# Optimization experiments

Measured on AMD Instinct MI355X. Metric: run time of the kernel, lower is better.

Reference implementation:

```python
import jax, jax.numpy as jnp
import numpy as np

B, C, N, H = 16, 256, 2048, 128


def setup_inputs() -> dict:
    key = jax.random.key(0)
    ks = jax.random.split(key, 9)
    s_in = 1.0 / np.sqrt(C)
    s_h = 1.0 / np.sqrt(H)
    return {
        "x": jax.random.normal(ks[0], (B, C, N), dtype=jnp.float32),
        "Wq": jax.random.uniform(ks[1], (H, C), jnp.float32, -s_in, s_in),
        "bq": jax.random.uniform(ks[2], (H,), jnp.float32, -s_in, s_in),
        "Wk": jax.random.uniform(ks[3], (H, C), jnp.float32, -s_in, s_in),
        "bk": jax.random.uniform(ks[4], (H,), jnp.float32, -s_in, s_in),
        "Wv": jax.random.uniform(ks[5], (H, C), jnp.float32, -s_in, s_in),
        "bv": jax.random.uniform(ks[6], (H,), jnp.float32, -s_in, s_in),
        "Wf": jax.random.uniform(ks[7], (C, H), jnp.float32, -s_h, s_h),
        "bf": jax.random.uniform(ks[8], (C,), jnp.float32, -s_h, s_h),
    }


def reference(x, Wq, bq, Wk, bk, Wv, bv, Wf, bf):
    # 1x1 conv == channel-wise linear: [B,C,N] -> [B,H,N]
    Q = jnp.einsum("bcn,hc->bhn", x, Wq) + bq[:, None]
    K = jnp.einsum("bcn,hc->bhn", x, Wk) + bk[:, None]
    V = jnp.einsum("bcn,hc->bhn", x, Wv) + bv[:, None]
    # attn[b, i, j] = softmax_j( Q[b,:,i] . K[b,:,j] )   (no sqrt(d) scaling, as in source)
    scores = jnp.einsum("bhi,bhj->bij", Q, K)          # [B, N, N]
    attn = jax.nn.softmax(scores, axis=-1)
    # out[b, h, i] = sum_j V[b,h,j] * attn[b,i,j]
    out = jnp.einsum("bhj,bij->bhi", V, attn)           # [B, H, N]
    out = jnp.einsum("bhn,ch->bcn", out, Wf) + bf[:, None]
    return out + x
```

## Files before the change

kernel.cpp:

```cpp
#include <hip/hip_runtime.h>
#include <hip/hip_bf16.h>

#define BATCH 16
#define CDIM 256
#define NDIM 2048
#define HDIM 128
#define KVB 64
#define NT (NDIM / KVB)

typedef __bf16 bf16;
typedef float f32x4 __attribute__((ext_vector_type(4)));
typedef float f32x16 __attribute__((ext_vector_type(16)));
typedef bf16 bf16x8 __attribute__((ext_vector_type(8)));
typedef unsigned int u32x4 __attribute__((ext_vector_type(4)));

#define LOG2E 1.4426950408889634f

__device__ __forceinline__ int swz512(int row, int colbyte) {
  return row * 512 + (colbyte ^ ((row & 15) << 4));
}
__device__ __forceinline__ int swz256(int row, int colbyte) {
  return row * 256 + (colbyte ^ ((row & 7) << 4));
}

__device__ __forceinline__ f32x4 mfma16(bf16x8 a, bf16x8 b, f32x4 c) {
  return __builtin_amdgcn_mfma_f32_16x16x32_bf16(a, b, c, 0, 0, 0);
}
__device__ __forceinline__ f32x16 mfma32(bf16x8 a, bf16x8 b, f32x16 c) {
  return __builtin_amdgcn_mfma_f32_32x32x16_bf16(a, b, c, 0, 0, 0);
}

__device__ __forceinline__ unsigned cvtpk(float lo, float hi) {
  unsigned r;
  asm("v_cvt_pk_bf16_f32 %0, %1, %2" : "=v"(r) : "v"(lo), "v"(hi));
  return r;
}
__device__ __forceinline__ void pswap(unsigned &a, unsigned &b) {
  asm volatile("v_permlane32_swap_b32 %0, %1" : "+v"(a), "+v"(b));
}

__device__ __forceinline__ void gload16(const bf16* g, char* l) {
  __builtin_amdgcn_global_load_lds(
      (const __attribute__((address_space(1))) void*)g,
      (__attribute__((address_space(3))) void*)l, 16, 0, 0);
}

__device__ __forceinline__ bf16x8 cvt8(float4 a, float4 b) {
  bf16x8 o;
  o[0] = (bf16)a.x; o[1] = (bf16)a.y; o[2] = (bf16)a.z; o[3] = (bf16)a.w;
  o[4] = (bf16)b.x; o[5] = (bf16)b.y; o[6] = (bf16)b.z; o[7] = (bf16)b.w;
  return o;
}

__global__ __launch_bounds__(256) void k1_qkv(
    const float* __restrict__ x,
    const float* __restrict__ Wq, const float* __restrict__ bq,
    const float* __restrict__ Wk, const float* __restrict__ bk,
    const float* __restrict__ Wv, const float* __restrict__ bv,
    bf16* __restrict__ Qo, bf16* __restrict__ Ko, bf16* __restrict__ Vo) {
  __shared__ char lds[65536];
  char* xT = lds;
  char* Wt = lds + 32768;

  const int t = threadIdx.x;
  const int l = t & 63;
  const int w = t >> 6;
  const int b = blockIdx.x >> 5;
  const int n0 = (blockIdx.x & 31) * 64;

#pragma unroll
  for (int pass = 0; pass < 16; ++pass) {
    int c = pass * 16 + (t >> 4);
    int nq = t & 15;
    const float4 v = *reinterpret_cast<const float4*>(
        x + (size_t)(b * CDIM + c) * NDIM + n0 + nq * 4);
    float fv[4] = {v.x, v.y, v.z, v.w};
#pragma unroll
    for (int i = 0; i < 4; ++i) {
      int row = nq * 4 + i;
      *reinterpret_cast<bf16*>(xT + swz512(row, c * 2)) = (bf16)fv[i];
    }
  }

  const float* Wp[3] = {Wq, Wk, Wv};
  const float* bp[3] = {bq, bk, bv};

#pragma unroll 1
  for (int p = 0; p < 3; ++p) {
    f32x4 acc[8];
#pragma unroll
    for (int i = 0; i < 8; ++i) acc[i] = f32x4{0.f, 0.f, 0.f, 0.f};

#pragma unroll 1
    for (int kh = 0; kh < 2; ++kh) {
      __syncthreads();
#pragma unroll
      for (int pass = 0; pass < 8; ++pass) {
        int h = pass * 16 + (t >> 4);
        int cq = t & 15;
        const float* src = Wp[p] + (size_t)h * CDIM + kh * 128 + cq * 8;
        float4 v0 = *reinterpret_cast<const float4*>(src);
        float4 v1 = *reinterpret_cast<const float4*>(src + 4);
        *reinterpret_cast<bf16x8*>(Wt + swz256(h, cq * 16)) = cvt8(v0, v1);
      }
      __syncthreads();

      if (p < 2) {
#pragma unroll
        for (int ks = 0; ks < 4; ++ks) {
          int cb2 = ks * 64 + (l >> 4) * 16;
          bf16x8 a = *reinterpret_cast<const bf16x8*>(
              xT + swz512(w * 16 + (l & 15), kh * 256 + cb2));
#pragma unroll
          for (int nf = 0; nf < 8; ++nf) {
            bf16x8 bb = *reinterpret_cast<const bf16x8*>(
                Wt + swz256(nf * 16 + (l & 15), cb2));
            acc[nf] = mfma16(a, bb, acc[nf]);
          }
        }
      } else {
#pragma unroll
        for (int ks = 0; ks < 4; ++ks) {
          int cb2 = ks * 64 + (l >> 4) * 16;
          bf16x8 a0 = *reinterpret_cast<const bf16x8*>(
              Wt + swz256(w * 32 + (l & 15), cb2));
          bf16x8 a1 = *reinterpret_cast<const bf16x8*>(
              Wt + swz256(w * 32 + 16 + (l & 15), cb2));
#pragma unroll
          for (int nf = 0; nf < 4; ++nf) {
            bf16x8 bb = *reinterpret_cast<const bf16x8*>(
                xT + swz512(nf * 16 + (l & 15), kh * 256 + cb2));
            acc[nf] = mfma16(a0, bb, acc[nf]);
            acc[4 + nf] = mfma16(a1, bb, acc[4 + nf]);
          }
        }
      }
    }

    if (p < 2) {
      bf16* dst = (p == 0) ? Qo : Ko;
#pragma unroll
      for (int nf = 0; nf < 8; ++nf) {
        float bias = bp[p][nf * 16 + (l & 15)];
#pragma unroll
        for (int r = 0; r < 4; ++r) {
          int n = n0 + w * 16 + (l >> 4) * 4 + r;
          int h = nf * 16 + (l & 15);
          dst[(size_t)(b * NDIM + n) * HDIM + h] = (bf16)(acc[nf][r] + bias);
        }
      }
    } else {
#pragma unroll
      for (int mf = 0; mf < 2; ++mf)
#pragma unroll
        for (int nf = 0; nf < 4; ++nf)
#pragma unroll
          for (int r = 0; r < 4; ++r) {
            int h = w * 32 + mf * 16 + (l >> 4) * 4 + r;
            int n = n0 + nf * 16 + (l & 15);
            Vo[(size_t)(b * HDIM + h) * NDIM + n] =
                (bf16)(acc[mf * 4 + nf][r] + bp[2][h]);
          }
    }
  }
}

__global__ __launch_bounds__(256, 2) void k2_attn(
    const bf16* __restrict__ Q, const bf16* __restrict__ K,
    const bf16* __restrict__ V, bf16* __restrict__ O) {
  extern __shared__ char lds[];

  const int t = threadIdx.x;
  const int l = t & 63;
  const int w = t >> 6;
  const int wm = w & 1;
  const int wk = w >> 1;
  const int hi = l >> 5;
  const int c31 = l & 31;

  const int pid = blockIdx.x;
  const int b = (pid & 7) * 2 + ((pid >> 3) >> 5);
  const int q0 = ((pid >> 3) & 31) * 64;

  bf16x8 qf[8];
  {
    const bf16* qb = Q + ((size_t)b * NDIM + q0 + wm * 32 + c31) * HDIM + hi * 8;
#pragma unroll
    for (int cs = 0; cs < 8; ++cs)
      qf[cs] = *reinterpret_cast<const bf16x8*>(qb + cs * 16);
  }

  unsigned offK[4], offV[4];
  {
    const int krow = w * 16 + (l >> 4);
    const int kslot = l & 15;
#pragma unroll
    for (int i = 0; i < 4; ++i) {
      int r = krow + i * 4;
      offK[i] = (unsigned)((b * NDIM + r) * HDIM + (kslot ^ (r & 15)) * 8);
    }
    const int vrow = w * 32 + (l >> 3);
    const int vslot = l & 7;
#pragma unroll
    for (int i = 0; i < 4; ++i) {
      int r = vrow + i * 8;
      offV[i] = (unsigned)((b * HDIM + r) * NDIM + (vslot ^ (r & 7)) * 8);
    }
  }
  const int kbase = w * 4096;
  const int vbase = 16384 + w * 4096;

  f32x16 oacc[4];
#pragma unroll
  for (int dg = 0; dg < 4; ++dg)
#pragma unroll
    for (int r = 0; r < 16; ++r) oacc[dg][r] = 0.f;
  float l_run = 0.f;

#pragma unroll
  for (int i = 0; i < 4; ++i) gload16(K + offK[i], lds + kbase + i * 1024);
#pragma unroll
  for (int i = 0; i < 4; ++i) gload16(V + offV[i], lds + vbase + i * 1024);

  const int krow = wk * 32 + c31;
  const int rxk = krow & 15;
  const int rxv = c31 & 7;

#pragma unroll 1
  for (int kt = 0; kt < NT; ++kt) {
    char* buf = lds + (kt & 1) * 32768;
    if (kt + 1 < NT) {
      char* nbuf = lds + ((kt + 1) & 1) * 32768;
#pragma unroll
      for (int i = 0; i < 4; ++i) {
        offK[i] += (unsigned)(KVB * HDIM);
        gload16(K + offK[i], nbuf + kbase + i * 1024);
      }
#pragma unroll
      for (int i = 0; i < 4; ++i) {
        offV[i] += (unsigned)KVB;
        gload16(V + offV[i], nbuf + vbase + i * 1024);
      }
      asm volatile("s_waitcnt vmcnt(8)" ::: "memory");
    } else {
      asm volatile("s_waitcnt vmcnt(0)" ::: "memory");
    }
    __builtin_amdgcn_s_barrier();

    const char* Kt = buf;
    const char* Vt = buf + 16384;

    f32x16 s;
#pragma unroll
    for (int r = 0; r < 16; ++r) s[r] = 0.f;
    __builtin_amdgcn_s_setprio(1);
    {
      const char* kr = Kt + krow * 256;
#pragma unroll
      for (int cs = 0; cs < 8; ++cs) {
        bf16x8 kf = *reinterpret_cast<const bf16x8*>(
            kr + (((cs * 2 + hi) ^ rxk) * 16));
        s = mfma32(kf, qf[cs], s);
      }
    }
    __builtin_amdgcn_s_setprio(0);

    float sum = 0.f;
#pragma unroll
    for (int r = 0; r < 16; ++r) {
      float p = __builtin_amdgcn_exp2f(s[r] * LOG2E);
      s[r] = p;
      sum += p;
    }
    l_run += sum;

    unsigned w0 = cvtpk(s[0], s[1]);
    unsigned w1 = cvtpk(s[2], s[3]);
    unsigned w2 = cvtpk(s[4], s[5]);
    unsigned w3 = cvtpk(s[6], s[7]);
    unsigned w4 = cvtpk(s[8], s[9]);
    unsigned w5 = cvtpk(s[10], s[11]);
    unsigned w6 = cvtpk(s[12], s[13]);
    unsigned w7 = cvtpk(s[14], s[15]);
    pswap(w0, w2); pswap(w1, w3); pswap(w4, w6); pswap(w5, w7);
    u32x4 pw0 = {w0, w1, w2, w3};
    u32x4 pw1 = {w4, w5, w6, w7};
    bf16x8 pa0 = __builtin_bit_cast(bf16x8, pw0);
    bf16x8 pa1 = __builtin_bit_cast(bf16x8, pw1);

    __builtin_amdgcn_s_setprio(1);
#pragma unroll
    for (int dg = 0; dg < 4; ++dg) {
      const char* vr = Vt + (dg * 32 + c31) * 128;
      bf16x8 vf0 = *reinterpret_cast<const bf16x8*>(
          vr + (((wk * 4 + 0 + hi) ^ rxv) * 16));
      oacc[dg] = mfma32(pa0, vf0, oacc[dg]);
      bf16x8 vf1 = *reinterpret_cast<const bf16x8*>(
          vr + (((wk * 4 + 2 + hi) ^ rxv) * 16));
      oacc[dg] = mfma32(pa1, vf1, oacc[dg]);
    }
    __builtin_amdgcn_s_setprio(0);
    __builtin_amdgcn_s_barrier();
  }

  l_run += __shfl_xor(l_run, 32);
  float* O1 = (float*)lds;
  float* L1 = (float*)(lds + 32768);
  if (wk == 1) {
#pragma unroll
    for (int dg = 0; dg < 4; ++dg)
#pragma unroll
      for (int r = 0; r < 16; ++r)
        O1[wm * 4096 + (dg * 16 + r) * 64 + l] = oacc[dg][r];
    if (l < 32) L1[wm * 32 + c31] = l_run;
  }
  __syncthreads();
  if (wk == 0) {
    float linv = 1.0f / (l_run + L1[wm * 32 + c31]);
    int ibits = __builtin_bit_cast(int, linv);
#pragma unroll
    for (int dg = 0; dg < 4; ++dg) {
      int h = dg * 32 + c31;
#pragma unroll
      for (int r = 0; r < 16; ++r) {
        int crow = (r & 3) + 8 * (r >> 2) + 4 * hi;
        float fr = __builtin_bit_cast(
            float, __builtin_amdgcn_ds_bpermute(crow * 4, ibits));
        float val = (oacc[dg][r] + O1[wm * 4096 + (dg * 16 + r) * 64 + l]) * fr;
        int n = q0 + wm * 32 + crow;
        O[((size_t)b * NDIM + n) * HDIM + h] = (bf16)val;
      }
    }
  }
}

__global__ __launch_bounds__(256) void k3_proj(
    const bf16* __restrict__ O, const float* __restrict__ Wf,
    const float* __restrict__ bfv, const float* __restrict__ x,
    float* __restrict__ out) {
  __shared__ char lds[49152];
  char* Wt = lds;
  char* Ot = lds + 32768;

  const int t = threadIdx.x;
  const int l = t & 63;
  const int w = t >> 6;
  const int b = blockIdx.x >> 5;
  const int n0 = (blockIdx.x & 31) * 64;

#pragma unroll
  for (int pass = 0; pass < 4; ++pass) {
    int n = pass * 16 + (t >> 4);
    int hq = t & 15;
    uint4 d = *reinterpret_cast<const uint4*>(
        O + (size_t)(b * NDIM + n0 + n) * HDIM + hq * 8);
    *reinterpret_cast<uint4*>(Ot + swz256(n, hq * 16)) = d;
  }

#pragma unroll 1
  for (int ch = 0; ch < 2; ++ch) {
    __syncthreads();
#pragma unroll
    for (int pass = 0; pass < 8; ++pass) {
      int cl = pass * 16 + (t >> 4);
      int hq = t & 15;
      const float* src = Wf + (size_t)(ch * 128 + cl) * HDIM + hq * 8;
      float4 v0 = *reinterpret_cast<const float4*>(src);
      float4 v1 = *reinterpret_cast<const float4*>(src + 4);
      *reinterpret_cast<bf16x8*>(Wt + swz256(cl, hq * 16)) = cvt8(v0, v1);
    }
    __syncthreads();

    f32x4 acc[2][4];
#pragma unroll
    for (int i = 0; i < 2; ++i)
#pragma unroll
      for (int j = 0; j < 4; ++j) acc[i][j] = f32x4{0.f, 0.f, 0.f, 0.f};

#pragma unroll
    for (int ks = 0; ks < 4; ++ks) {
      int cb = ks * 64 + (l >> 4) * 16;
      bf16x8 a0 = *reinterpret_cast<const bf16x8*>(
          Wt + swz256(w * 32 + (l & 15), cb));
      bf16x8 a1 = *reinterpret_cast<const bf16x8*>(
          Wt + swz256(w * 32 + 16 + (l & 15), cb));
#pragma unroll
      for (int nf = 0; nf < 4; ++nf) {
        bf16x8 bb = *reinterpret_cast<const bf16x8*>(
            Ot + swz256(nf * 16 + (l & 15), cb));
        acc[0][nf] = mfma16(a0, bb, acc[0][nf]);
        acc[1][nf] = mfma16(a1, bb, acc[1][nf]);
      }
    }

#pragma unroll
    for (int mf = 0; mf < 2; ++mf)
#pragma unroll
      for (int nf = 0; nf < 4; ++nf)
#pragma unroll
        for (int r = 0; r < 4; ++r) {
          int c = ch * 128 + w * 32 + mf * 16 + (l >> 4) * 4 + r;
          int n = n0 + nf * 16 + (l & 15);
          size_t idx = (size_t)(b * CDIM + c) * NDIM + n;
          out[idx] = acc[mf][nf][r] + bfv[c] + x[idx];
        }
  }
}

extern "C" void kernel_launch(void* const* d_in, const int* in_sizes, int n_in,
                              void* d_out, int out_size, void* d_ws,
                              size_t ws_size, hipStream_t stream) {
  (void)in_sizes; (void)n_in; (void)out_size;
  const float* x = (const float*)d_in[0];
  const float* Wq = (const float*)d_in[1];
  const float* bq = (const float*)d_in[2];
  const float* Wk = (const float*)d_in[3];
  const float* bk = (const float*)d_in[4];
  const float* Wv = (const float*)d_in[5];
  const float* bv = (const float*)d_in[6];
  const float* Wf = (const float*)d_in[7];
  const float* bfv = (const float*)d_in[8];
  float* out = (float*)d_out;

  if (ws_size < (24u << 20)) return;
  char* ws = (char*)d_ws;
  bf16* Qb = (bf16*)(ws);
  bf16* Kb = (bf16*)(ws + (8u << 20));
  bf16* Vb = (bf16*)(ws + (16u << 20));

  const unsigned k2_lds = 65536;
  hipFuncSetAttribute(reinterpret_cast<const void*>(k2_attn),
                      hipFuncAttributeMaxDynamicSharedMemorySize, (int)k2_lds);

  k1_qkv<<<512, 256, 0, stream>>>(x, Wq, bq, Wk, bk, Wv, bv, Qb, Kb, Vb);
  k2_attn<<<512, 256, k2_lds, stream>>>(Qb, Kb, Vb, Qb);
  k3_proj<<<512, 256, 0, stream>>>(Qb, Wf, bfv, x, out);
}
```

Baseline: 95.46 us.

## Pre-pack QKV weights into MFMA fragments and fuse three projections in one pass

Adds a small prep kernel that converts Wq/Wk/Wv to bf16 in MFMA fragment order, stored in scratch at the tail of the output buffer. The QKV kernel then reads these fragments directly from global memory and computes Q, K and V in a single loop over channels, removing per-projection LDS weight staging and barriers. The x transpose into LDS now uses lane shuffles and packed writes. The log2(e) scale is folded into Q so the attention softmax skips a multiply per score. It adds an extra launch and reuses the output buffer as temporary storage, and the Q rounding to bf16 now happens after scaling.

```diff
diff --git a/kernel.cpp b/kernel.cpp
--- a/kernel.cpp
+++ b/kernel.cpp
@@ -13,6 +13,7 @@
 typedef float f32x16 __attribute__((ext_vector_type(16)));
 typedef bf16 bf16x8 __attribute__((ext_vector_type(8)));
 typedef unsigned int u32x4 __attribute__((ext_vector_type(4)));
+typedef unsigned int u32x2 __attribute__((ext_vector_type(2)));
 
 #define LOG2E 1.4426950408889634f
 
@@ -52,117 +53,111 @@
   return o;
 }
 
-__global__ __launch_bounds__(256) void k1_qkv(
-    const float* __restrict__ x,
-    const float* __restrict__ Wq, const float* __restrict__ bq,
-    const float* __restrict__ Wk, const float* __restrict__ bk,
-    const float* __restrict__ Wv, const float* __restrict__ bv,
+__global__ __launch_bounds__(256) void k0_prep(
+    const float* __restrict__ Wq, const float* __restrict__ Wk,
+    const float* __restrict__ Wv, bf16* __restrict__ blk) {
+  int tg = blockIdx.x * 256 + threadIdx.x;
+  int f = tg >> 6, l = tg & 63;
+  const float* W = (f < 64) ? Wq : (f < 128 ? Wk : Wv);
+  int ks = (f >> 3) & 7, hb = f & 7;
+  const float* src = W + (size_t)(hb * 16 + (l & 15)) * CDIM + ks * 32 + (l >> 4) * 8;
+  float4 v0 = *reinterpret_cast<const float4*>(src);
+  float4 v1 = *reinterpret_cast<const float4*>(src + 4);
+  *reinterpret_cast<bf16x8*>(blk + f * 512 + l * 8) = cvt8(v0, v1);
+}
+
+__global__ __launch_bounds__(256, 3) void k1_qkv(
+    const float* __restrict__ x, const bf16* __restrict__ blk,
+    const float* __restrict__ bq, const float* __restrict__ bk,
+    const float* __restrict__ bv,
     bf16* __restrict__ Qo, bf16* __restrict__ Ko, bf16* __restrict__ Vo) {
-  __shared__ char lds[65536];
-  char* xT = lds;
-  char* Wt = lds + 32768;
+  __shared__ char xT[32768];
 
   const int t = threadIdx.x;
   const int l = t & 63;
   const int w = t >> 6;
+  const int q = (l >> 4) & 3;
   const int b = blockIdx.x >> 5;
   const int n0 = (blockIdx.x & 31) * 64;
 
 #pragma unroll
-  for (int pass = 0; pass < 16; ++pass) {
-    int c = pass * 16 + (t >> 4);
-    int nq = t & 15;
-    const float4 v = *reinterpret_cast<const float4*>(
-        x + (size_t)(b * CDIM + c) * NDIM + n0 + nq * 4);
-    float fv[4] = {v.x, v.y, v.z, v.w};
-#pragma unroll
-    for (int i = 0; i < 4; ++i) {
-      int row = nq * 4 + i;
-      *reinterpret_cast<bf16*>(xT + swz512(row, c * 2)) = (bf16)fv[i];
-    }
-  }
-
-  const float* Wp[3] = {Wq, Wk, Wv};
-  const float* bp[3] = {bq, bk, bv};
-
-#pragma unroll 1
-  for (int p = 0; p < 3; ++p) {
-    f32x4 acc[8];
-#pragma unroll
-    for (int i = 0; i < 8; ++i) acc[i] = f32x4{0.f, 0.f, 0.f, 0.f};
-
-#pragma unroll 1
-    for (int kh = 0; kh < 2; ++kh) {
-      __syncthreads();
-#pragma unroll
-      for (int pass = 0; pass < 8; ++pass) {
-        int h = pass * 16 + (t >> 4);
-        int cq = t & 15;
-        const float* src = Wp[p] + (size_t)h * CDIM + kh * 128 + cq * 8;
-        float4 v0 = *reinterpret_cast<const float4*>(src);
-        float4 v1 = *reinterpret_cast<const float4*>(src + 4);
-        *reinterpret_cast<bf16x8*>(Wt + swz256(h, cq * 16)) = cvt8(v0, v1);
-      }
-      __syncthreads();
-
-      if (p < 2) {
-#pragma unroll
-        for (int ks = 0; ks < 4; ++ks) {
-          int cb2 = ks * 64 + (l >> 4) * 16;
-          bf16x8 a = *reinterpret_cast<const bf16x8*>(
-              xT + swz512(w * 16 + (l & 15), kh * 256 + cb2));
-#pragma unroll
-          for (int nf = 0; nf < 8; ++nf) {
-            bf16x8 bb = *reinterpret_cast<const bf16x8*>(
-                Wt + swz256(nf * 16 + (l & 15), cb2));
-            acc[nf] = mfma16(a, bb, acc[nf]);
-          }
-        }
-      } else {
-#pragma unroll
-        for (int ks = 0; ks < 4; ++ks) {
-          int cb2 = ks * 64 + (l >> 4) * 16;
-          bf16x8 a0 = *reinterpret_cast<const bf16x8*>(
-              Wt + swz256(w * 32 + (l & 15), cb2));
-          bf16x8 a1 = *reinterpret_cast<const bf16x8*>(
-              Wt + swz256(w * 32 + 16 + (l & 15), cb2));
-#pragma unroll
-          for (int nf = 0; nf < 4; ++nf) {
-            bf16x8 bb = *reinterpret_cast<const bf16x8*>(
-                xT + swz512(nf * 16 + (l & 15), kh * 256 + cb2));
-            acc[nf] = mfma16(a0, bb, acc[nf]);
-            acc[4 + nf] = mfma16(a1, bb, acc[4 + nf]);
-          }
-        }
-      }
-    }
-
-    if (p < 2) {
-      bf16* dst = (p == 0) ? Qo : Ko;
-#pragma unroll
-      for (int nf = 0; nf < 8; ++nf) {
-        float bias = bp[p][nf * 16 + (l & 15)];
-#pragma unroll
-        for (int r = 0; r < 4; ++r) {
-          int n = n0 + w * 16 + (l >> 4) * 4 + r;
-          int h = nf * 16 + (l & 15);
-          dst[(size_t)(b * NDIM + n) * HDIM + h] = (bf16)(acc[nf][r] + bias);
-        }
-      }
-    } else {
-#pragma unroll
-      for (int mf = 0; mf < 2; ++mf)
-#pragma unroll
-        for (int nf = 0; nf < 4; ++nf)
-#pragma unroll
-          for (int r = 0; r < 4; ++r) {
-            int h = w * 32 + mf * 16 + (l >> 4) * 4 + r;
-            int n = n0 + nf * 16 + (l & 15);
-            Vo[(size_t)(b * HDIM + h) * NDIM + n] =
-                (bf16)(acc[mf * 4 + nf][r] + bp[2][h]);
-          }
-    }
-  }
+  for (int p = 0; p < 16; ++p) {
+    int c = w * 64 + p * 4 + q;
+    float4 v = *reinterpret_cast<const float4*>(
+        x + (size_t)(b * CDIM + c) * NDIM + n0 + (l & 15) * 4);
+    float t0 = __shfl_xor(v.x, 16), t1 = __shfl_xor(v.y, 16);
+    float t2 = __shfl_xor(v.z, 16), t3 = __shfl_xor(v.w, 16);
+    float4 wv;
+    if ((q & 1) == 0) wv = make_float4(v.x, t0, v.z, t2);
+    else              wv = make_float4(t1, v.y, t3, v.w);
+    float s0 = __shfl_xor(wv.x, 32), s1 = __shfl_xor(wv.y, 32);
+    float s2 = __shfl_xor(wv.z, 32), s3 = __shfl_xor(wv.w, 32);
+    float4 z;
+    if ((q & 2) == 0) z = make_float4(wv.x, wv.y, s0, s1);
+    else              z = make_float4(s2, s3, wv.z, wv.w);
+    u32x2 pk = {cvtpk(z.x, z.y), cvtpk(z.z, z.w)};
+    int n = (l & 15) * 4 + q;
+    int slot = w * 8 + (p >> 1);
+    *reinterpret_cast<u32x2*>(
+        xT + n * 512 + ((slot ^ (n & 15)) * 16 + (p & 1) * 8)) = pk;
+  }
+  __syncthreads();
+
+  const bf16* bq_ = blk;
+  const bf16* bk_ = blk + 64 * 512;
+  const bf16* bv_ = blk + 128 * 512;
+
+  f32x4 aq[8], ak[8], av[8];
+#pragma unroll
+  for (int i = 0; i < 8; ++i) {
+    aq[i] = f32x4{0.f, 0.f, 0.f, 0.f};
+    ak[i] = f32x4{0.f, 0.f, 0.f, 0.f};
+    av[i] = f32x4{0.f, 0.f, 0.f, 0.f};
+  }
+
+#pragma unroll
+  for (int ks = 0; ks < 8; ++ks) {
+    bf16x8 a = *reinterpret_cast<const bf16x8*>(
+        xT + swz512(w * 16 + (l & 15), ks * 64 + (l >> 4) * 16));
+#pragma unroll
+    for (int nf = 0; nf < 8; ++nf) {
+      bf16x8 wq = *reinterpret_cast<const bf16x8*>(bq_ + (ks * 8 + nf) * 512 + l * 8);
+      aq[nf] = mfma16(a, wq, aq[nf]);
+      bf16x8 wk = *reinterpret_cast<const bf16x8*>(bk_ + (ks * 8 + nf) * 512 + l * 8);
+      ak[nf] = mfma16(a, wk, ak[nf]);
+    }
+    bf16x8 wv0 = *reinterpret_cast<const bf16x8*>(bv_ + (ks * 8 + w * 2 + 0) * 512 + l * 8);
+    bf16x8 wv1 = *reinterpret_cast<const bf16x8*>(bv_ + (ks * 8 + w * 2 + 1) * 512 + l * 8);
+#pragma unroll
+    for (int nf4 = 0; nf4 < 4; ++nf4) {
+      bf16x8 bx = *reinterpret_cast<const bf16x8*>(
+          xT + swz512(nf4 * 16 + (l & 15), ks * 64 + (l >> 4) * 16));
+      av[nf4] = mfma16(wv0, bx, av[nf4]);
+      av[4 + nf4] = mfma16(wv1, bx, av[4 + nf4]);
+    }
+  }
+
+#pragma unroll
+  for (int nf = 0; nf < 8; ++nf) {
+    int h = nf * 16 + (l & 15);
+    float biasq = bq[h], biask = bk[h];
+#pragma unroll
+    for (int r = 0; r < 4; ++r) {
+      int n = n0 + w * 16 + (l >> 4) * 4 + r;
+      Qo[(size_t)(b * NDIM + n) * HDIM + h] = (bf16)((aq[nf][r] + biasq) * LOG2E);
+      Ko[(size_t)(b * NDIM + n) * HDIM + h] = (bf16)(ak[nf][r] + biask);
+    }
+  }
+#pragma unroll
+  for (int mf = 0; mf < 2; ++mf)
+#pragma unroll
+    for (int nf4 = 0; nf4 < 4; ++nf4)
+#pragma unroll
+      for (int r = 0; r < 4; ++r) {
+        int h = w * 32 + mf * 16 + (l >> 4) * 4 + r;
+        int n = n0 + nf4 * 16 + (l & 15);
+        Vo[(size_t)(b * HDIM + h) * NDIM + n] = (bf16)(av[mf * 4 + nf4][r] + bv[h]);
+      }
 }
 
 __global__ __launch_bounds__(256, 2) void k2_attn(
@@ -268,7 +263,7 @@
     float sum = 0.f;
 #pragma unroll
     for (int r = 0; r < 16; ++r) {
-      float p = __builtin_amdgcn_exp2f(s[r] * LOG2E);
+      float p = __builtin_amdgcn_exp2f(s[r]);
       s[r] = p;
       sum += p;
     }
@@ -410,7 +405,7 @@
 extern "C" void kernel_launch(void* const* d_in, const int* in_sizes, int n_in,
                               void* d_out, int out_size, void* d_ws,
                               size_t ws_size, hipStream_t stream) {
-  (void)in_sizes; (void)n_in; (void)out_size;
+  (void)in_sizes; (void)n_in;
   const float* x = (const float*)d_in[0];
   const float* Wq = (const float*)d_in[1];
   const float* bq = (const float*)d_in[2];
@@ -428,11 +423,15 @@
   bf16* Kb = (bf16*)(ws + (8u << 20));
   bf16* Vb = (bf16*)(ws + (16u << 20));
 
+  const size_t out_bytes = (size_t)out_size * 4;
+  bf16* Wblk = (bf16*)((char*)d_out + out_bytes - 196608);
+
   const unsigned k2_lds = 65536;
   hipFuncSetAttribute(reinterpret_cast<const void*>(k2_attn),
                       hipFuncAttributeMaxDynamicSharedMemorySize, (int)k2_lds);
 
-  k1_qkv<<<512, 256, 0, stream>>>(x, Wq, bq, Wk, bk, Wv, bv, Qb, Kb, Vb);
+  k0_prep<<<48, 256, 0, stream>>>(Wq, Wk, Wv, Wblk);
+  k1_qkv<<<512, 256, 0, stream>>>(x, Wblk, bq, bk, bv, Qb, Kb, Vb);
   k2_attn<<<512, 256, k2_lds, stream>>>(Qb, Kb, Vb, Qb);
   k3_proj<<<512, 256, 0, stream>>>(Qb, Wf, bfv, x, out);
 }
```

Measured after the change: 110.9 us. 1.16x slower.

## Fold log2e into Q, prefetch V before exp, and vectorize x transpose

Applied to the files above, without the earlier changes.

Q is now scaled by log2(e) when it is written in the projection kernel, so the attention loop can call exp2 directly without a per-element multiply. The V fragments are loaded from LDS before the exponentials so the load latency overlaps the exp work, and the row sum uses a tree reduction. The x transpose into LDS now uses cross-lane shuffles so each thread writes packed 8-byte bf16 stores instead of scattered 2-byte stores. Rounding Q to bf16 after scaling changes numerics slightly, and holding eight V fragments raises register pressure.

```diff
diff --git a/kernel.cpp b/kernel.cpp
--- a/kernel.cpp
+++ b/kernel.cpp
@@ -13,6 +13,7 @@
 typedef float f32x16 __attribute__((ext_vector_type(16)));
 typedef bf16 bf16x8 __attribute__((ext_vector_type(8)));
 typedef unsigned int u32x4 __attribute__((ext_vector_type(4)));
+typedef unsigned int u32x2 __attribute__((ext_vector_type(2)));
 
 #define LOG2E 1.4426950408889634f
 
@@ -65,21 +66,30 @@
   const int t = threadIdx.x;
   const int l = t & 63;
   const int w = t >> 6;
+  const int q = (l >> 4) & 3;
   const int b = blockIdx.x >> 5;
   const int n0 = (blockIdx.x & 31) * 64;
 
 #pragma unroll
-  for (int pass = 0; pass < 16; ++pass) {
-    int c = pass * 16 + (t >> 4);
-    int nq = t & 15;
-    const float4 v = *reinterpret_cast<const float4*>(
-        x + (size_t)(b * CDIM + c) * NDIM + n0 + nq * 4);
-    float fv[4] = {v.x, v.y, v.z, v.w};
-#pragma unroll
-    for (int i = 0; i < 4; ++i) {
-      int row = nq * 4 + i;
-      *reinterpret_cast<bf16*>(xT + swz512(row, c * 2)) = (bf16)fv[i];
-    }
+  for (int p = 0; p < 16; ++p) {
+    int c = w * 64 + p * 4 + q;
+    float4 v = *reinterpret_cast<const float4*>(
+        x + (size_t)(b * CDIM + c) * NDIM + n0 + (l & 15) * 4);
+    float t0 = __shfl_xor(v.x, 16), t1 = __shfl_xor(v.y, 16);
+    float t2 = __shfl_xor(v.z, 16), t3 = __shfl_xor(v.w, 16);
+    float4 wv;
+    if ((q & 1) == 0) wv = make_float4(v.x, t0, v.z, t2);
+    else              wv = make_float4(t1, v.y, t3, v.w);
+    float s0 = __shfl_xor(wv.x, 32), s1 = __shfl_xor(wv.y, 32);
+    float s2 = __shfl_xor(wv.z, 32), s3 = __shfl_xor(wv.w, 32);
+    float4 z;
+    if ((q & 2) == 0) z = make_float4(wv.x, wv.y, s0, s1);
+    else              z = make_float4(s2, s3, wv.z, wv.w);
+    u32x2 pk = {cvtpk(z.x, z.y), cvtpk(z.z, z.w)};
+    int n = (l & 15) * 4 + q;
+    int slot = w * 8 + (p >> 1);
+    *reinterpret_cast<u32x2*>(
+        xT + n * 512 + ((slot ^ (n & 15)) * 16 + (p & 1) * 8)) = pk;
   }
 
   const float* Wp[3] = {Wq, Wk, Wv};
@@ -139,6 +149,7 @@
 
     if (p < 2) {
       bf16* dst = (p == 0) ? Qo : Ko;
+      const float scale = (p == 0) ? LOG2E : 1.0f;
 #pragma unroll
       for (int nf = 0; nf < 8; ++nf) {
         float bias = bp[p][nf * 16 + (l & 15)];
@@ -146,7 +157,7 @@
         for (int r = 0; r < 4; ++r) {
           int n = n0 + w * 16 + (l >> 4) * 4 + r;
           int h = nf * 16 + (l & 15);
-          dst[(size_t)(b * NDIM + n) * HDIM + h] = (bf16)(acc[nf][r] + bias);
+          dst[(size_t)(b * NDIM + n) * HDIM + h] = (bf16)((acc[nf][r] + bias) * scale);
         }
       }
     } else {
@@ -265,14 +276,24 @@
     }
     __builtin_amdgcn_s_setprio(0);
 
-    float sum = 0.f;
-#pragma unroll
-    for (int r = 0; r < 16; ++r) {
-      float p = __builtin_amdgcn_exp2f(s[r] * LOG2E);
-      s[r] = p;
-      sum += p;
-    }
-    l_run += sum;
+    bf16x8 vf[8];
+#pragma unroll
+    for (int dg = 0; dg < 4; ++dg) {
+      const char* vr = Vt + (dg * 32 + c31) * 128;
+      vf[2 * dg + 0] = *reinterpret_cast<const bf16x8*>(
+          vr + (((wk * 4 + 0 + hi) ^ rxv) * 16));
+      vf[2 * dg + 1] = *reinterpret_cast<const bf16x8*>(
+          vr + (((wk * 4 + 2 + hi) ^ rxv) * 16));
+    }
+
+#pragma unroll
+    for (int r = 0; r < 16; ++r) s[r] = __builtin_amdgcn_exp2f(s[r]);
+    {
+      float a0 = s[0] + s[1], a1 = s[2] + s[3], a2 = s[4] + s[5], a3 = s[6] + s[7];
+      float a4 = s[8] + s[9], a5 = s[10] + s[11], a6 = s[12] + s[13], a7 = s[14] + s[15];
+      float b0 = a0 + a1, b1 = a2 + a3, b2 = a4 + a5, b3 = a6 + a7;
+      l_run += (b0 + b1) + (b2 + b3);
+    }
 
     unsigned w0 = cvtpk(s[0], s[1]);
     unsigned w1 = cvtpk(s[2], s[3]);
@@ -291,13 +312,8 @@
     __builtin_amdgcn_s_setprio(1);
 #pragma unroll
     for (int dg = 0; dg < 4; ++dg) {
-      const char* vr = Vt + (dg * 32 + c31) * 128;
-      bf16x8 vf0 = *reinterpret_cast<const bf16x8*>(
-          vr + (((wk * 4 + 0 + hi) ^ rxv) * 16));
-      oacc[dg] = mfma32(pa0, vf0, oacc[dg]);
-      bf16x8 vf1 = *reinterpret_cast<const bf16x8*>(
-          vr + (((wk * 4 + 2 + hi) ^ rxv) * 16));
-      oacc[dg] = mfma32(pa1, vf1, oacc[dg]);
+      oacc[dg] = mfma32(pa0, vf[2 * dg + 0], oacc[dg]);
+      oacc[dg] = mfma32(pa1, vf[2 * dg + 1], oacc[dg]);
     }
     __builtin_amdgcn_s_setprio(0);
     __builtin_amdgcn_s_barrier();
```

Result: slower. 98.71 us (+3.4%).
